# Performance work log

Hardware: AMD Instinct MI355X
Metric: run time of the kernel (lower is better)

## Reference

```python
import jax, jax.numpy as jnp
import numpy as np

B, T, N, FIN, FOUT, EDGE_DIM = 8, 16, 256, 32, 32, 16


def setup_inputs() -> dict:
    key = jax.random.key(0)
    ks = jax.random.split(key, 8)
    def xavier(k, shape):
        fan_in, fan_out = shape[0], shape[1]
        limit = float(np.sqrt(6.0 / (fan_in + fan_out)))
        return jax.random.uniform(k, shape, jnp.float32, -limit, limit)
    return {
        "x": jax.random.normal(ks[0], (B, T, N, FIN), jnp.float32),
        "adj": jax.random.uniform(ks[1], (N, N), jnp.float32),
        # edge_net: Linear(1, edge_dim) -> GELU -> Linear(edge_dim, Fin*Fout)
        "w1": xavier(ks[2], (1, EDGE_DIM)),
        "b1": jnp.zeros((EDGE_DIM,), jnp.float32),
        "w2": xavier(ks[3], (EDGE_DIM, FIN * FOUT)),
        "b2": jnp.zeros((FIN * FOUT,), jnp.float32),
        # node_lin: Linear(Fin, Fout)
        "node_w": xavier(ks[4], (FIN, FOUT)),
        "node_b": jnp.zeros((FOUT,), jnp.float32),
    }


def reference(x, adj, w1, b1, w2, b2, node_w, node_b):
    # edge-conditioned weights: (N, N, Fin, Fout)
    h = jax.nn.gelu(adj[:, :, None] * w1[0] + b1, approximate=False)  # (N,N,E)
    edge_w = (h @ w2 + b2).reshape(N, N, FIN, FOUT)
    # msg[b,t,i,j,:] = sum_f x[b,t,j,f] * edge_w[i,j,f,:]; agg = sum_j msg
    agg = jnp.einsum("btjf,ijfo->btio", x, edge_w)  # (B,T,N,Fout)
    y = jax.nn.gelu(x @ node_w + node_b + agg, approximate=False)
    return y
```

## Files before the change

kernel.cpp:

```cpp
#include <hip/hip_runtime.h>
#include <math.h>

#define NB    256
#define FINN  32
#define FOUTN 32
#define BT    128


typedef __attribute__((ext_vector_type(8))) short short8;
typedef __attribute__((ext_vector_type(4))) float floatx4;

#define MFMA16(a,b,c) __builtin_amdgcn_mfma_f32_16x16x32_bf16((a),(b),(c),0,0,0)

#define BARRIER() asm volatile("s_waitcnt lgkmcnt(0)\n\ts_barrier" ::: "memory")

__device__ __forceinline__ float gelu_f(float v) {
    return 0.5f * v * (1.0f + erff(v * 0.70710678118654752f));
}
__device__ __forceinline__ ushort f2bf(float x) {
    union { float f; unsigned u; } v; v.f = x;
    unsigned r = (v.u + 0x7FFFu + ((v.u >> 16) & 1u)) >> 16;
    return (ushort)r;
}
__device__ __forceinline__ uint2 pack4(floatx4 d) {
    uint2 p;
    p.x = (unsigned)f2bf(d[0]) | ((unsigned)f2bf(d[1]) << 16);
    p.y = (unsigned)f2bf(d[2]) | ((unsigned)f2bf(d[3]) << 16);
    return p;
}

__global__ __launch_bounds__(256) void prep_kernel(
        const float* __restrict__ x,   const float* __restrict__ adj,
        const float* __restrict__ w1,  const float* __restrict__ b1,
        const float* __restrict__ w2,  const float* __restrict__ b2,
        const float* __restrict__ node_w, const float* __restrict__ node_b,
        ushort* __restrict__ Hf, ushort* __restrict__ w2f,
        ushort* __restrict__ xaf, ushort* __restrict__ nwf,
        float* __restrict__ bias2g) {
    int bid = blockIdx.x;
    int tid = threadIdx.x;

    if (bid < 128) {
        __shared__ float adjs[16][264];
        __shared__ float w1s[16], b1s[16];
        int it = bid & 15;
        int kq8 = bid >> 4;
        if (tid < 16) { w1s[tid] = w1[tid]; b1s[tid] = b1[tid]; }
        #pragma unroll
        for (int q = 0; q < 4; ++q) {
            int u = q * 256 + tid;
            int row = u >> 6, c4 = u & 63;
            *(float4*)&adjs[row][c4 * 4] =
                ((const float4*)(adj + ((size_t)it * 16 + row) * 256))[c4];
        }
        __syncthreads();
        #pragma unroll
        for (int q = 0; q < 4; ++q) {
            int u = q * 256 + tid;
            int ks = kq8 * 16 + (u >> 6);
            int lane = u & 63;
            int m = lane & 15, quad = lane >> 4;
            int e = ks >> 3;
            int j0 = (ks & 7) * 32 + quad * 8;
            float w = w1s[e], b = b1s[e];
            ushort tmp[8];
            #pragma unroll
            for (int d = 0; d < 8; ++d)
                tmp[d] = f2bf(gelu_f(adjs[m][j0 + d] * w + b));
            *(int4*)(Hf + (((size_t)it * 128 + ks) * 64 + lane) * 8) = *(int4*)tmp;
        }
        return;
    }
    if (bid < 160) {
        int wv = tid >> 6, lane = tid & 63, m = lane & 15, quad = lane >> 4;
        int bt = (bid - 128) * 4 + wv;
        #pragma unroll
        for (int jt = 0; jt < 16; ++jt) {
            const float* xs = x + ((size_t)bt * NB + jt * 16 + m) * FINN + quad * 8;
            float4 lo = *(const float4*)xs;
            float4 hi = *(const float4*)(xs + 4);
            ushort tmp[8];
            tmp[0]=f2bf(lo.x); tmp[1]=f2bf(lo.y); tmp[2]=f2bf(lo.z); tmp[3]=f2bf(lo.w);
            tmp[4]=f2bf(hi.x); tmp[5]=f2bf(hi.y); tmp[6]=f2bf(hi.z); tmp[7]=f2bf(hi.w);
            *(int4*)(xaf + (((size_t)bt * 16 + jt) * 64 + lane) * 8) = *(int4*)tmp;
        }
        return;
    }
    if (bid < 288) {
        __shared__ float Sp[8][32];
        __shared__ float Svs[32];
        int bt = bid - 160;
        int f = tid & 31, grp = tid >> 5;
        float s = 0.f;
        for (int j = grp; j < NB; j += 8)
            s += x[((size_t)bt * NB + j) * FINN + f];
        Sp[grp][f] = s;
        __syncthreads();
        if (tid < 32) {
            float s2 = 0.f;
            #pragma unroll
            for (int g = 0; g < 8; ++g) s2 += Sp[g][tid];
            Svs[tid] = s2;
        }
        __syncthreads();
        if (tid < 32) {
            float bb = node_b[tid];
            #pragma unroll
            for (int f2 = 0; f2 < FINN; ++f2)
                bb += Svs[f2] * b2[f2 * FOUTN + tid];
            bias2g[bt * 32 + tid] = bb;
        }
        return;
    }
    for (int s = 0; s < 2048; s += 256) {
        int slot = s + tid;
        int e = slot >> 7, r = slot & 127;
        int ot = r >> 6, lane = r & 63;
        int m = lane & 15, quad = lane >> 4;
        const float* src = w2 + (size_t)e * 1024 + (quad * 8) * 32 + ot * 16 + m;
        ushort tmp[8];
        #pragma unroll
        for (int i = 0; i < 8; ++i) tmp[i] = f2bf(src[i * 32]);
        *(int4*)(w2f + (size_t)slot * 8) = *(int4*)tmp;
    }
    if (tid < 128) {
        int ot = tid >> 6, lane = tid & 63, m = lane & 15, q = lane >> 4;
        ushort tmp[8];
        #pragma unroll
        for (int d = 0; d < 8; ++d)
            tmp[d] = f2bf(node_w[(q * 8 + d) * 32 + ot * 16 + m]);
        *(int4*)(nwf + tid * 8) = *(int4*)tmp;
    }
}

__global__ __launch_bounds__(1024, 4) void main_kernel(
        const ushort* __restrict__ Hf,  const ushort* __restrict__ w2f,
        const ushort* __restrict__ xaf, float* __restrict__ Cp) {
    __shared__ ushort Bsl[2][8][2][512];

    int bt   = blockIdx.x;
    int kq   = blockIdx.y;
    int tid  = threadIdx.x;
    int wv   = tid >> 6;
    int lane = tid & 63;
    int m    = lane & 15;
    int quad = lane >> 4;

    short8 xfr = *(const short8*)(xaf + (((size_t)bt * 16 + wv) * 64 + lane) * 8);
    const int qc  = (wv & 1) * 2 + (quad >> 1);
    const int dp  = (quad & 1) * 4;
    const int jp0 = wv >> 1;

    const ushort* Ha = Hf + (size_t)wv * 128 * 512 + (size_t)lane * 8;
    const ushort* Wl = w2f + (size_t)lane * 8;

    short8 areg[8];
    floatx4 acc[2] = {};

    #define ALOAD(slot, s_)                                                   \
    {                                                                         \
        int ks_ = kq * 32 + (s_); if (ks_ > 127) ks_ = 127;                   \
        areg[slot] = *(const short8*)(Ha + (size_t)ks_ * 512);                \
    }
    #define PRODUCE(bp, wf0, wf1)                                             \
    {                                                                         \
        floatx4 z = {0.f, 0.f, 0.f, 0.f};                                     \
        floatx4 d0 = MFMA16(xfr, wf0, z);                                     \
        floatx4 d1 = MFMA16(xfr, wf1, z);                                     \
        *(uint2*)((bp) + jp0 * 1024 +       (qc * 16 + m) * 8 + dp) = pack4(d0); \
        *(uint2*)((bp) + jp0 * 1024 + 512 + (qc * 16 + m) * 8 + dp) = pack4(d1); \
    }

    #pragma unroll
    for (int s = 0; s < 8; ++s) ALOAD(s, s);
    {
        short8 wf0 = *(const short8*)(Wl + (size_t)(kq * 4) * 1024);
        short8 wf1 = *(const short8*)(Wl + (size_t)(kq * 4) * 1024 + 512);
        PRODUCE((ushort*)Bsl, wf0, wf1);
    }
    BARRIER();

    #pragma unroll 1
    for (int w = 0; w < 4; ++w) {
        int en = kq * 4 + ((w < 3) ? (w + 1) : 3);
        short8 wf0 = *(const short8*)(Wl + (size_t)en * 1024);
        short8 wf1 = *(const short8*)(Wl + (size_t)en * 1024 + 512);

        ushort* Bb = (ushort*)Bsl + (w & 1) * 8192;
        #pragma unroll
        for (int kk = 0; kk < 8; ++kk) {
            short8 a = areg[kk];
            ALOAD(kk, w * 8 + kk + 8);
            short8 b0 = *(const short8*)(Bb + kk * 1024 + lane * 8);
            short8 b1 = *(const short8*)(Bb + kk * 1024 + 512 + lane * 8);
            acc[0] = MFMA16(a, b0, acc[0]);
            acc[1] = MFMA16(a, b1, acc[1]);
        }
        if (w < 3) {
            ushort* Bn = (ushort*)Bsl + ((w + 1) & 1) * 8192;
            PRODUCE(Bn, wf0, wf1);
        }
        BARRIER();
    }

    #pragma unroll
    for (int oh = 0; oh < 2; ++oh)
        #pragma unroll
        for (int r = 0; r < 4; ++r) {
            int i = wv * 16 + quad * 4 + r;
            Cp[(((size_t)bt * NB + i) * 4 + kq) * FOUTN + oh * 16 + m]
                = acc[oh][r];
        }
    #undef ALOAD
    #undef PRODUCE
}

__global__ __launch_bounds__(256) void epi_kernel(
        const ushort* __restrict__ xaf, const ushort* __restrict__ nwf,
        const float* __restrict__ bias2g, const float* __restrict__ Cp,
        float* __restrict__ out) {
    int bt   = blockIdx.x;
    int ih   = blockIdx.y;
    int tid  = threadIdx.x;
    int wv   = tid >> 6;
    int lane = tid & 63;
    int m    = lane & 15;
    int quad = lane >> 4;

    short8 nb0 = *(const short8*)(nwf + (size_t)lane * 8);
    short8 nb1 = *(const short8*)(nwf + ((size_t)64 + lane) * 8);

    #pragma unroll
    for (int t = 0; t < 2; ++t) {
        int it = ih * 8 + wv * 2 + t;
        short8 xa = *(const short8*)(xaf + (((size_t)bt * 16 + it) * 64 + lane) * 8);
        #pragma unroll
        for (int tn = 0; tn < 2; ++tn) {
            floatx4 z = {0.f, 0.f, 0.f, 0.f};
            floatx4 ea = MFMA16(xa, tn ? nb1 : nb0, z);
            float bz = bias2g[bt * 32 + tn * 16 + m];
            #pragma unroll
            for (int r = 0; r < 4; ++r) {
                int i = it * 16 + quad * 4 + r;
                float s = ea[r] + bz;
                #pragma unroll
                for (int kqi = 0; kqi < 4; ++kqi)
                    s += Cp[(((size_t)bt * NB + i) * 4 + kqi) * FOUTN + tn * 16 + m];
                out[((size_t)bt * NB + i) * FOUTN + tn * 16 + m] = gelu_f(s);
            }
        }
    }
}

extern "C" void kernel_launch(void* const* d_in, const int* in_sizes, int n_in,
                              void* d_out, int out_size, void* d_ws, size_t ws_size,
                              hipStream_t stream) {
    const float* x      = (const float*)d_in[0];
    const float* adj    = (const float*)d_in[1];
    const float* w1     = (const float*)d_in[2];
    const float* b1     = (const float*)d_in[3];
    const float* w2     = (const float*)d_in[4];
    const float* b2     = (const float*)d_in[5];
    const float* node_w = (const float*)d_in[6];
    const float* node_b = (const float*)d_in[7];
    float* out = (float*)d_out;

    ushort* Hf     = (ushort*)d_ws;
    ushort* w2f    = Hf + (size_t)16 * 128 * 512;
    ushort* xaf    = w2f + 16384;
    ushort* nwf    = xaf + (size_t)128 * 16 * 512;
    float*  bias2g = (float*)(nwf + 1024);
    float*  Cp     = bias2g + 128 * 32;

    hipLaunchKernelGGL(prep_kernel, dim3(289), dim3(256), 0, stream,
                       x, adj, w1, b1, w2, b2, node_w, node_b,
                       Hf, w2f, xaf, nwf, bias2g);
    hipLaunchKernelGGL(main_kernel, dim3(BT, 4), dim3(1024), 0, stream,
                       Hf, w2f, xaf, Cp);
    hipLaunchKernelGGL(epi_kernel, dim3(BT, 2), dim3(256), 0, stream,
                       xaf, nwf, bias2g, Cp, out);
}
```

Measured before the change: 106.1 us.

## Retile main kernel so each block covers two bt and two row tiles

The main GEMM kernel is retiled. Each 512-thread block now handles two batch-time slices and two 16-row tiles per wave, with the K split widened from 4 to 8 parts. Every H A-fragment loaded from global memory now feeds four MFMAs instead of two, and each produced B tile in LDS is reused across both row tiles. This cuts global traffic for H. The cost is twice as many partial sums written to and read back from Cp in the epilogue, plus more register pressure from the larger accumulators.

```diff
diff --git a/kernel.cpp b/kernel.cpp
--- a/kernel.cpp
+++ b/kernel.cpp
@@ -133,84 +133,93 @@
     }
 }
 
-__global__ __launch_bounds__(1024, 4) void main_kernel(
+__global__ __launch_bounds__(512, 4) void main_kernel(
         const ushort* __restrict__ Hf,  const ushort* __restrict__ w2f,
         const ushort* __restrict__ xaf, float* __restrict__ Cp) {
-    __shared__ ushort Bsl[2][8][2][512];
-
-    int bt   = blockIdx.x;
-    int kq   = blockIdx.y;
+    __shared__ ushort Bsl[2][2][8][2][512];
+
+    int btg  = blockIdx.x;
+    int eq   = blockIdx.y;
     int tid  = threadIdx.x;
     int wv   = tid >> 6;
     int lane = tid & 63;
     int m    = lane & 15;
     int quad = lane >> 4;
 
-    short8 xfr = *(const short8*)(xaf + (((size_t)bt * 16 + wv) * 64 + lane) * 8);
-    const int qc  = (wv & 1) * 2 + (quad >> 1);
-    const int dp  = (quad & 1) * 4;
-    const int jp0 = wv >> 1;
-
-    const ushort* Ha = Hf + (size_t)wv * 128 * 512 + (size_t)lane * 8;
-    const ushort* Wl = w2f + (size_t)lane * 8;
-
-    short8 areg[8];
-    floatx4 acc[2] = {};
+    int pbt = wv & 1, jq = wv >> 1;
+    short8 xfr[4];
+    #pragma unroll
+    for (int q = 0; q < 4; ++q)
+        xfr[q] = *(const short8*)(xaf +
+            (((size_t)(btg * 2 + pbt) * 16 + jq * 4 + q) * 64 + lane) * 8);
+
+    const ushort* Ha0 = Hf + (size_t)(wv    ) * 128 * 512 + (size_t)lane * 8;
+    const ushort* Ha1 = Hf + (size_t)(wv + 8) * 128 * 512 + (size_t)lane * 8;
+    const ushort* Wl  = w2f + (size_t)lane * 8;
+
+    short8 areg[4][2];
+    floatx4 acc[2][2][2] = {};
 
     #define ALOAD(slot, s_)                                                   \
     {                                                                         \
-        int ks_ = kq * 32 + (s_); if (ks_ > 127) ks_ = 127;                   \
-        areg[slot] = *(const short8*)(Ha + (size_t)ks_ * 512);                \
-    }
-    #define PRODUCE(bp, wf0, wf1)                                             \
+        int ks_ = eq * 16 + (s_); if (ks_ > 127) ks_ = 127;                   \
+        areg[slot][0] = *(const short8*)(Ha0 + (size_t)ks_ * 512);            \
+        areg[slot][1] = *(const short8*)(Ha1 + (size_t)ks_ * 512);            \
+    }
+    #define PRODUCE(buf, e_)                                                  \
     {                                                                         \
-        floatx4 z = {0.f, 0.f, 0.f, 0.f};                                     \
-        floatx4 d0 = MFMA16(xfr, wf0, z);                                     \
-        floatx4 d1 = MFMA16(xfr, wf1, z);                                     \
-        *(uint2*)((bp) + jp0 * 1024 +       (qc * 16 + m) * 8 + dp) = pack4(d0); \
-        *(uint2*)((bp) + jp0 * 1024 + 512 + (qc * 16 + m) * 8 + dp) = pack4(d1); \
+        short8 wf0 = *(const short8*)(Wl + (size_t)(e_) * 1024);              \
+        short8 wf1 = *(const short8*)(Wl + (size_t)(e_) * 1024 + 512);        \
+        _Pragma("unroll")                                                     \
+        for (int q = 0; q < 4; ++q) {                                         \
+            int jp = jq * 2 + (q >> 1);                                       \
+            int qc = (q & 1) * 2 + (quad >> 1);                               \
+            int dp = (quad & 1) * 4;                                          \
+            floatx4 z = {0.f, 0.f, 0.f, 0.f};                                 \
+            floatx4 d0 = MFMA16(xfr[q], wf0, z);                              \
+            floatx4 d1 = MFMA16(xfr[q], wf1, z);                              \
+            *(uint2*)&Bsl[buf][pbt][jp][0][(qc * 16 + m) * 8 + dp] = pack4(d0); \
+            *(uint2*)&Bsl[buf][pbt][jp][1][(qc * 16 + m) * 8 + dp] = pack4(d1); \
+        }                                                                     \
+    }
+
+    ALOAD(0, 0); ALOAD(1, 1); ALOAD(2, 2); ALOAD(3, 3);
+    PRODUCE(0, eq * 2);
+    BARRIER();
+
+    #pragma unroll 1
+    for (int w = 0; w < 2; ++w) {
+        if (w == 0) PRODUCE(1, eq * 2 + 1);
+        #pragma unroll
+        for (int kk = 0; kk < 8; ++kk) {
+            short8 a0 = areg[kk & 3][0];
+            short8 a1 = areg[kk & 3][1];
+            ALOAD(kk & 3, w * 8 + kk + 4);
+            #pragma unroll
+            for (int bb = 0; bb < 2; ++bb)
+                #pragma unroll
+                for (int oh = 0; oh < 2; ++oh) {
+                    short8 b = *(const short8*)&Bsl[w & 1][bb][kk][oh][lane * 8];
+                    acc[0][bb][oh] = MFMA16(a0, b, acc[0][bb][oh]);
+                    acc[1][bb][oh] = MFMA16(a1, b, acc[1][bb][oh]);
+                }
+        }
+        BARRIER();
     }
 
     #pragma unroll
-    for (int s = 0; s < 8; ++s) ALOAD(s, s);
-    {
-        short8 wf0 = *(const short8*)(Wl + (size_t)(kq * 4) * 1024);
-        short8 wf1 = *(const short8*)(Wl + (size_t)(kq * 4) * 1024 + 512);
-        PRODUCE((ushort*)Bsl, wf0, wf1);
-    }
-    BARRIER();
-
-    #pragma unroll 1
-    for (int w = 0; w < 4; ++w) {
-        int en = kq * 4 + ((w < 3) ? (w + 1) : 3);
-        short8 wf0 = *(const short8*)(Wl + (size_t)en * 1024);
-        short8 wf1 = *(const short8*)(Wl + (size_t)en * 1024 + 512);
-
-        ushort* Bb = (ushort*)Bsl + (w & 1) * 8192;
-        #pragma unroll
-        for (int kk = 0; kk < 8; ++kk) {
-            short8 a = areg[kk];
-            ALOAD(kk, w * 8 + kk + 8);
-            short8 b0 = *(const short8*)(Bb + kk * 1024 + lane * 8);
-            short8 b1 = *(const short8*)(Bb + kk * 1024 + 512 + lane * 8);
-            acc[0] = MFMA16(a, b0, acc[0]);
-            acc[1] = MFMA16(a, b1, acc[1]);
-        }
-        if (w < 3) {
-            ushort* Bn = (ushort*)Bsl + ((w + 1) & 1) * 8192;
-            PRODUCE(Bn, wf0, wf1);
-        }
-        BARRIER();
-    }
-
-    #pragma unroll
-    for (int oh = 0; oh < 2; ++oh)
-        #pragma unroll
-        for (int r = 0; r < 4; ++r) {
-            int i = wv * 16 + quad * 4 + r;
-            Cp[(((size_t)bt * NB + i) * 4 + kq) * FOUTN + oh * 16 + m]
-                = acc[oh][r];
-        }
+    for (int t = 0; t < 2; ++t)
+        #pragma unroll
+        for (int bb = 0; bb < 2; ++bb)
+            #pragma unroll
+            for (int oh = 0; oh < 2; ++oh)
+                #pragma unroll
+                for (int r = 0; r < 4; ++r) {
+                    int i = (wv + 8 * t) * 16 + quad * 4 + r;
+                    int bt = btg * 2 + bb;
+                    Cp[(((size_t)bt * NB + i) * 8 + eq) * FOUTN + oh * 16 + m]
+                        = acc[t][bb][oh][r];
+                }
     #undef ALOAD
     #undef PRODUCE
 }
@@ -244,8 +253,8 @@
                 int i = it * 16 + quad * 4 + r;
                 float s = ea[r] + bz;
                 #pragma unroll
-                for (int kqi = 0; kqi < 4; ++kqi)
-                    s += Cp[(((size_t)bt * NB + i) * 4 + kqi) * FOUTN + tn * 16 + m];
+                for (int kqi = 0; kqi < 8; ++kqi)
+                    s += Cp[(((size_t)bt * NB + i) * 8 + kqi) * FOUTN + tn * 16 + m];
                 out[((size_t)bt * NB + i) * FOUTN + tn * 16 + m] = gelu_f(s);
             }
         }
@@ -275,7 +284,7 @@
     hipLaunchKernelGGL(prep_kernel, dim3(289), dim3(256), 0, stream,
                        x, adj, w1, b1, w2, b2, node_w, node_b,
                        Hf, w2f, xaf, nwf, bias2g);
-    hipLaunchKernelGGL(main_kernel, dim3(BT, 4), dim3(1024), 0, stream,
+    hipLaunchKernelGGL(main_kernel, dim3(64, 8), dim3(512), 0, stream,
                        Hf, w2f, xaf, Cp);
     hipLaunchKernelGGL(epi_kernel, dim3(BT, 2), dim3(256), 0, stream,
                        xaf, nwf, bias2g, Cp, out);
```

Result: no change. 107.7 us (+1.6%).

## Fuse main and epilogue kernels with full-K per-block accumulation

Applied to the files above, without the earlier changes.

Replaces the split-K main kernel plus separate epilogue with a single fused kernel. Each 128-thread block now covers two 16-row output tiles across the full K range, so the partial-sum buffer Cp is gone. The node-linear term, bias and GELU are applied directly from accumulators. This removes one launch and the Cp global round trip. In exchange, blocks are much smaller and each runs a longer sequential K loop with double-buffered LDS and many barriers, which may lower per-CU parallelism.

```diff
diff --git a/kernel.cpp b/kernel.cpp
--- a/kernel.cpp
+++ b/kernel.cpp
@@ -133,92 +133,12 @@
     }
 }
 
-__global__ __launch_bounds__(1024, 4) void main_kernel(
+__global__ __launch_bounds__(128, 4) void fused_kernel(
         const ushort* __restrict__ Hf,  const ushort* __restrict__ w2f,
-        const ushort* __restrict__ xaf, float* __restrict__ Cp) {
-    __shared__ ushort Bsl[2][8][2][512];
-
-    int bt   = blockIdx.x;
-    int kq   = blockIdx.y;
-    int tid  = threadIdx.x;
-    int wv   = tid >> 6;
-    int lane = tid & 63;
-    int m    = lane & 15;
-    int quad = lane >> 4;
-
-    short8 xfr = *(const short8*)(xaf + (((size_t)bt * 16 + wv) * 64 + lane) * 8);
-    const int qc  = (wv & 1) * 2 + (quad >> 1);
-    const int dp  = (quad & 1) * 4;
-    const int jp0 = wv >> 1;
-
-    const ushort* Ha = Hf + (size_t)wv * 128 * 512 + (size_t)lane * 8;
-    const ushort* Wl = w2f + (size_t)lane * 8;
-
-    short8 areg[8];
-    floatx4 acc[2] = {};
-
-    #define ALOAD(slot, s_)                                                   \
-    {                                                                         \
-        int ks_ = kq * 32 + (s_); if (ks_ > 127) ks_ = 127;                   \
-        areg[slot] = *(const short8*)(Ha + (size_t)ks_ * 512);                \
-    }
-    #define PRODUCE(bp, wf0, wf1)                                             \
-    {                                                                         \
-        floatx4 z = {0.f, 0.f, 0.f, 0.f};                                     \
-        floatx4 d0 = MFMA16(xfr, wf0, z);                                     \
-        floatx4 d1 = MFMA16(xfr, wf1, z);                                     \
-        *(uint2*)((bp) + jp0 * 1024 +       (qc * 16 + m) * 8 + dp) = pack4(d0); \
-        *(uint2*)((bp) + jp0 * 1024 + 512 + (qc * 16 + m) * 8 + dp) = pack4(d1); \
-    }
-
-    #pragma unroll
-    for (int s = 0; s < 8; ++s) ALOAD(s, s);
-    {
-        short8 wf0 = *(const short8*)(Wl + (size_t)(kq * 4) * 1024);
-        short8 wf1 = *(const short8*)(Wl + (size_t)(kq * 4) * 1024 + 512);
-        PRODUCE((ushort*)Bsl, wf0, wf1);
-    }
-    BARRIER();
-
-    #pragma unroll 1
-    for (int w = 0; w < 4; ++w) {
-        int en = kq * 4 + ((w < 3) ? (w + 1) : 3);
-        short8 wf0 = *(const short8*)(Wl + (size_t)en * 1024);
-        short8 wf1 = *(const short8*)(Wl + (size_t)en * 1024 + 512);
-
-        ushort* Bb = (ushort*)Bsl + (w & 1) * 8192;
-        #pragma unroll
-        for (int kk = 0; kk < 8; ++kk) {
-            short8 a = areg[kk];
-            ALOAD(kk, w * 8 + kk + 8);
-            short8 b0 = *(const short8*)(Bb + kk * 1024 + lane * 8);
-            short8 b1 = *(const short8*)(Bb + kk * 1024 + 512 + lane * 8);
-            acc[0] = MFMA16(a, b0, acc[0]);
-            acc[1] = MFMA16(a, b1, acc[1]);
-        }
-        if (w < 3) {
-            ushort* Bn = (ushort*)Bsl + ((w + 1) & 1) * 8192;
-            PRODUCE(Bn, wf0, wf1);
-        }
-        BARRIER();
-    }
-
-    #pragma unroll
-    for (int oh = 0; oh < 2; ++oh)
-        #pragma unroll
-        for (int r = 0; r < 4; ++r) {
-            int i = wv * 16 + quad * 4 + r;
-            Cp[(((size_t)bt * NB + i) * 4 + kq) * FOUTN + oh * 16 + m]
-                = acc[oh][r];
-        }
-    #undef ALOAD
-    #undef PRODUCE
-}
-
-__global__ __launch_bounds__(256) void epi_kernel(
         const ushort* __restrict__ xaf, const ushort* __restrict__ nwf,
-        const float* __restrict__ bias2g, const float* __restrict__ Cp,
-        float* __restrict__ out) {
+        const float* __restrict__ bias2g, float* __restrict__ out) {
+    __shared__ ushort Bsl[2][4][2][512];
+
     int bt   = blockIdx.x;
     int ih   = blockIdx.y;
     int tid  = threadIdx.x;
@@ -226,30 +146,115 @@
     int lane = tid & 63;
     int m    = lane & 15;
     int quad = lane >> 4;
-
-    short8 nb0 = *(const short8*)(nwf + (size_t)lane * 8);
-    short8 nb1 = *(const short8*)(nwf + ((size_t)64 + lane) * 8);
-
+    int it   = ih * 2 + wv;
+
+    short8 xfr[2][2][2];
     #pragma unroll
-    for (int t = 0; t < 2; ++t) {
-        int it = ih * 8 + wv * 2 + t;
+    for (int h = 0; h < 2; ++h)
+        #pragma unroll
+        for (int c = 0; c < 2; ++c)
+            #pragma unroll
+            for (int d = 0; d < 2; ++d)
+                xfr[h][c][d] = *(const short8*)(xaf +
+                    (((size_t)bt * 16 + h * 8 + 4 * wv + 2 * c + d) * 64 + lane) * 8);
+
+    const ushort* Ha = Hf + (size_t)it * 128 * 512 + (size_t)lane * 8;
+    const ushort* Wl = w2f + (size_t)lane * 8;
+
+    short8 areg[2][4];
+    short8 wr[2][2];
+    floatx4 acc[2] = {};
+
+    #define ALOADW(p, wnext)                                                  \
+    {                                                                         \
+        int ksb = (wnext) * 4;                                                \
+        _Pragma("unroll")                                                     \
+        for (int kk = 0; kk < 4; ++kk) {                                      \
+            int ks = ksb + kk; if (ks > 127) ks = 127;                        \
+            areg[p][kk] = *(const short8*)(Ha + (size_t)ks * 512);            \
+        }                                                                     \
+    }
+    #define WLOAD(p, e_)                                                      \
+    {                                                                         \
+        int ec = (e_) > 15 ? 15 : (e_);                                       \
+        wr[p][0] = *(const short8*)(Wl + (size_t)ec * 1024);                  \
+        wr[p][1] = *(const short8*)(Wl + (size_t)ec * 1024 + 512);            \
+    }
+    #define PRODUCE(bp, hp, ep)                                               \
+    {                                                                         \
+        _Pragma("unroll")                                                     \
+        for (int c = 0; c < 2; ++c) {                                         \
+            int kk = 2 * wv + c;                                              \
+            _Pragma("unroll")                                                 \
+            for (int d = 0; d < 2; ++d) {                                     \
+                int qc = d * 2 + (quad >> 1);                                 \
+                int dp = (quad & 1) * 4;                                      \
+                floatx4 z = {0.f, 0.f, 0.f, 0.f};                             \
+                floatx4 d0 = MFMA16(xfr[hp][c][d], wr[ep][0], z);             \
+                floatx4 d1 = MFMA16(xfr[hp][c][d], wr[ep][1], z);             \
+                *(uint2*)&Bsl[bp][kk][0][(qc * 16 + m) * 8 + dp] = pack4(d0); \
+                *(uint2*)&Bsl[bp][kk][1][(qc * 16 + m) * 8 + dp] = pack4(d1); \
+            }                                                                 \
+        }                                                                     \
+    }
+    #define CONSUME(bp, ap)                                                   \
+    {                                                                         \
+        _Pragma("unroll")                                                     \
+        for (int kk = 0; kk < 4; ++kk) {                                      \
+            short8 b0 = *(const short8*)&Bsl[bp][kk][0][lane * 8];            \
+            short8 b1 = *(const short8*)&Bsl[bp][kk][1][lane * 8];            \
+            acc[0] = MFMA16(areg[ap][kk], b0, acc[0]);                        \
+            acc[1] = MFMA16(areg[ap][kk], b1, acc[1]);                        \
+        }                                                                     \
+    }
+
+    ALOADW(0, 0);
+    WLOAD(0, 0);
+    WLOAD(1, 1);
+    PRODUCE(0, 0, 0);
+    BARRIER();
+
+    #pragma unroll 1
+    for (int ww = 0; ww < 8; ++ww) {
+        ALOADW(1, 4 * ww + 1);
+        PRODUCE(1, 1, 0);
+        CONSUME(0, 0);
+        BARRIER();
+        ALOADW(0, 4 * ww + 2);
+        PRODUCE(0, 0, 1);
+        CONSUME(1, 1);
+        WLOAD(0, 2 * ww + 2);
+        BARRIER();
+        ALOADW(1, 4 * ww + 3);
+        PRODUCE(1, 1, 1);
+        CONSUME(0, 0);
+        BARRIER();
+        ALOADW(0, 4 * ww + 4);
+        PRODUCE(0, 0, 0);
+        CONSUME(1, 1);
+        WLOAD(1, 2 * ww + 3);
+        BARRIER();
+    }
+
+    {
         short8 xa = *(const short8*)(xaf + (((size_t)bt * 16 + it) * 64 + lane) * 8);
         #pragma unroll
-        for (int tn = 0; tn < 2; ++tn) {
-            floatx4 z = {0.f, 0.f, 0.f, 0.f};
-            floatx4 ea = MFMA16(xa, tn ? nb1 : nb0, z);
-            float bz = bias2g[bt * 32 + tn * 16 + m];
+        for (int oh = 0; oh < 2; ++oh) {
+            short8 nb = *(const short8*)(nwf + ((size_t)oh * 64 + lane) * 8);
+            acc[oh] = MFMA16(xa, nb, acc[oh]);
+            float bz = bias2g[bt * 32 + oh * 16 + m];
             #pragma unroll
             for (int r = 0; r < 4; ++r) {
                 int i = it * 16 + quad * 4 + r;
-                float s = ea[r] + bz;
-                #pragma unroll
-                for (int kqi = 0; kqi < 4; ++kqi)
-                    s += Cp[(((size_t)bt * NB + i) * 4 + kqi) * FOUTN + tn * 16 + m];
-                out[((size_t)bt * NB + i) * FOUTN + tn * 16 + m] = gelu_f(s);
+                out[((size_t)bt * NB + i) * FOUTN + oh * 16 + m]
+                    = gelu_f(acc[oh][r] + bz);
             }
         }
     }
+    #undef ALOADW
+    #undef WLOAD
+    #undef PRODUCE
+    #undef CONSUME
 }
 
 extern "C" void kernel_launch(void* const* d_in, const int* in_sizes, int n_in,
@@ -270,13 +275,10 @@
     ushort* xaf    = w2f + 16384;
     ushort* nwf    = xaf + (size_t)128 * 16 * 512;
     float*  bias2g = (float*)(nwf + 1024);
-    float*  Cp     = bias2g + 128 * 32;
 
     hipLaunchKernelGGL(prep_kernel, dim3(289), dim3(256), 0, stream,
                        x, adj, w1, b1, w2, b2, node_w, node_b,
                        Hf, w2f, xaf, nwf, bias2g);
-    hipLaunchKernelGGL(main_kernel, dim3(BT, 4), dim3(1024), 0, stream,
-                       Hf, w2f, xaf, Cp);
-    hipLaunchKernelGGL(epi_kernel, dim3(BT, 2), dim3(256), 0, stream,
-                       xaf, nwf, bias2g, Cp, out);
-}
+    hipLaunchKernelGGL(fused_kernel, dim3(BT, 8), dim3(128), 0, stream,
+                       Hf, w2f, xaf, nwf, bias2g, out);
+}
```

Result: no change. 107.3 us (+1.2%).
